# Performance work log

Measured on AMD Instinct MI355X. Metric: run time of the kernel, lower is better.

The kernel has to match this reference:

```python
import jax, jax.numpy as jnp
import numpy as np

B, T, HID, H = 2, 2048, 2048, 8
DK, DV = 256, 512          # head_qk_dim, head_v_dim
CHUNK = 64                 # chunk size used by fused_chunk retention
EPS = 1e-5


def setup_inputs() -> dict:
    key = jax.random.key(0)
    ks = jax.random.split(key, 7)
    s = 0.02  # ~ xavier_uniform with gain 2**-2.5
    return {
        "hidden_states": jax.random.normal(ks[0], (B, T, HID), jnp.float32),
        "Wq": jax.random.normal(ks[1], (HID, H * DK), jnp.float32) * s,
        "Wk": jax.random.normal(ks[2], (HID, H * DK), jnp.float32) * s,
        "Wv": jax.random.normal(ks[3], (HID, H * DV), jnp.float32) * s,
        "Wg": jax.random.normal(ks[4], (HID, H * DV), jnp.float32) * s,
        "Wo": jax.random.normal(ks[5], (H * DV, HID), jnp.float32) * s,
        "g_norm_w": jnp.ones((DV,), jnp.float32),
    }


def _rotary(x):
    # x: [B, T, H, D], non-interleaved rotary over full head dim, base 10000
    d = x.shape[-1]
    inv = 1.0 / (10000.0 ** (jnp.arange(0, d, 2, dtype=jnp.float32) / d))
    fr = jnp.arange(x.shape[1], dtype=jnp.float32)[:, None] * inv  # [T, d/2]
    cos = jnp.cos(fr)[None, :, None, :]
    sin = jnp.sin(fr)[None, :, None, :]
    x1, x2 = jnp.split(x, 2, axis=-1)
    return jnp.concatenate([x1 * cos - x2 * sin, x2 * cos + x1 * sin], axis=-1)


def _retention(q, k, v):
    # q,k: [B,H,T,DK]; v: [B,H,T,DV]; per-head decay gamma_h = 1 - 2^(-5-h)
    gamma = 1.0 - jnp.exp2(-5.0 - jnp.arange(H, dtype=jnp.float32))  # [H]
    q = q * (DK ** -0.5)
    N = T // CHUNK
    qc = q.reshape(B, H, N, CHUNK, DK).transpose(2, 0, 1, 3, 4)  # [N,B,H,C,K]
    kc = k.reshape(B, H, N, CHUNK, DK).transpose(2, 0, 1, 3, 4)
    vc = v.reshape(B, H, N, CHUNK, DV).transpose(2, 0, 1, 3, 4)
    i = jnp.arange(CHUNK, dtype=jnp.float32)
    # intra-chunk causal decay matrix D[h,i,j] = gamma_h^(i-j) for i>=j else 0
    Dm = jnp.where(i[:, None] >= i[None, :],
                   gamma[:, None, None] ** (i[:, None] - i[None, :]), 0.0)  # [H,C,C]
    qd = gamma[:, None] ** (i + 1.0)            # [H,C]: decay applied to q vs carried state
    kd = gamma[:, None] ** (CHUNK - 1.0 - i)    # [H,C]: decay applied to k for state update
    gC = gamma ** CHUNK                          # [H]

    def step(S, qkv):
        qcu, kcu, vcu = qkv  # [B,H,C,K], [B,H,C,K], [B,H,C,V]
        A = jnp.einsum('bhik,bhjk->bhij', qcu, kcu) * Dm[None]
        o_intra = jnp.einsum('bhij,bhjv->bhiv', A, vcu)
        o_inter = jnp.einsum('bhck,bhkv->bhcv', qcu * qd[None, :, :, None], S)
        kv = jnp.einsum('bhck,bhcv->bhkv', kcu * kd[None, :, :, None], vcu)
        S_new = gC[None, :, None, None] * S + kv
        return S_new, o_intra + o_inter

    S0 = jnp.zeros((B, H, DK, DV), jnp.float32)
    _, o = jax.lax.scan(step, S0, (qc, kc, vc))  # o: [N,B,H,C,V]
    return o.transpose(1, 2, 0, 3, 4).reshape(B, H, T, DV)


def reference(hidden_states, Wq, Wk, Wv, Wg, Wo, g_norm_w):
    q = (hidden_states @ Wq).reshape(B, T, H, DK)
    k = (hidden_states @ Wk).reshape(B, T, H, DK)
    v = (hidden_states @ Wv).reshape(B, T, H, DV)
    q = _rotary(q)
    k = _rotary(k)
    o = _retention(q.transpose(0, 2, 1, 3), k.transpose(0, 2, 1, 3),
                   v.transpose(0, 2, 1, 3))          # [B,H,T,DV]
    o = o.transpose(0, 2, 1, 3)                       # [B,T,H,DV]
    g = (hidden_states @ Wg).reshape(B, T, H, DV)
    # fused RMSNorm (per head_v_dim) + swish gate
    o = o * jax.lax.rsqrt(jnp.mean(o * o, axis=-1, keepdims=True) + EPS) * g_norm_w
    o = o * (g * jax.nn.sigmoid(g))
    return o.reshape(B, T, H * DV) @ Wo
```

## Files before the change

kernel.cpp:

```cpp
#include <hip/hip_runtime.h>
#include <cstdint>
#include <cstddef>

typedef __bf16 bf16;
typedef __bf16 bf16x8 __attribute__((ext_vector_type(8)));
typedef float  f32x4  __attribute__((ext_vector_type(4)));

#define MFMA16(a, b, c) __builtin_amdgcn_mfma_f32_16x16x32_bf16((a), (b), (c), 0, 0, 0)

__device__ __forceinline__ void async16(const bf16* g, bf16* l) {
  __builtin_amdgcn_global_load_lds(
      (const __attribute__((address_space(1))) unsigned int*)g,
      (__attribute__((address_space(3))) unsigned int*)l, 16, 0, 0);
}

__global__ __launch_bounds__(256) void k_cast(const float* __restrict__ x, bf16* __restrict__ y) {
  size_t i = ((size_t)blockIdx.x * 256 + threadIdx.x) * 4;
  float4 a = *(const float4*)(x + i);
  union { bf16 h[4]; uint2 u; } pk;
  pk.h[0] = (bf16)a.x; pk.h[1] = (bf16)a.y; pk.h[2] = (bf16)a.z; pk.h[3] = (bf16)a.w;
  *(uint2*)(y + i) = pk.u;
}

__global__ __launch_bounds__(256) void k_wt_all(const float* __restrict__ Wq,
                                                const float* __restrict__ Wk,
                                                const float* __restrict__ Wv,
                                                const float* __restrict__ Wg,
                                                bf16* __restrict__ WT) {
  const int K = 2048;
  __shared__ float tile[32][33];
  int z = blockIdx.z;
  const float* W; bf16* dst; int N;
  if (z == 0)      { W = Wq; dst = WT;                          N = 2048; }
  else if (z == 1) { W = Wk; dst = WT + (size_t)2048 * 2048;    N = 2048; }
  else if (z == 2) { W = Wv; dst = WT + (size_t)4096 * 2048;    N = 4096; }
  else             { W = Wg; dst = WT + (size_t)8192 * 2048;    N = 4096; }
  int n0 = blockIdx.x << 5;
  if (n0 >= N) return;
  int k0 = blockIdx.y << 5;
  int r = threadIdx.x >> 5, c = threadIdx.x & 31;
#pragma unroll
  for (int p = 0; p < 4; p++)
    tile[r + p * 8][c] = W[(size_t)(k0 + r + p * 8) * N + n0 + c];
  __syncthreads();
#pragma unroll
  for (int p = 0; p < 4; p++) {
    int nn = r + p * 8;
    dst[(size_t)(n0 + nn) * K + k0 + c] = (bf16)tile[c][nn];
  }
}

__global__ __launch_bounds__(256) void k_transpose_cast(const float* __restrict__ W,
                                                        bf16* __restrict__ WT, int K, int N) {
  __shared__ float tile[32][33];
  int k0 = blockIdx.y << 5, n0 = blockIdx.x << 5;
  int r = threadIdx.x >> 5, c = threadIdx.x & 31;
#pragma unroll
  for (int p = 0; p < 4; p++)
    tile[r + p * 8][c] = W[(size_t)(k0 + r + p * 8) * N + n0 + c];
  __syncthreads();
#pragma unroll
  for (int p = 0; p < 4; p++) {
    int nn = r + p * 8;
    WT[(size_t)(n0 + nn) * K + k0 + c] = (bf16)tile[c][nn];
  }
}

__global__ __launch_bounds__(256) void k_transpose_bh(const bf16* __restrict__ src,
                                                      bf16* __restrict__ dst, int D) {
  __shared__ bf16 tile[32][33];
  int bh = blockIdx.z;
  int b = bh >> 3, h = bh & 7;
  int d0 = blockIdx.x << 5, t0 = blockIdx.y << 5;
  int r = threadIdx.x >> 5, c = threadIdx.x & 31;
#pragma unroll
  for (int p = 0; p < 4; p++)
    tile[r + p * 8][c] = src[((size_t)((b * 2048 + t0 + r + p * 8) * 8 + h)) * D + d0 + c];
  __syncthreads();
#pragma unroll
  for (int p = 0; p < 4; p++)
    dst[((size_t)(bh * D + d0 + r + p * 8)) * 2048 + t0 + c] = tile[c][r + p * 8];
}

__global__ __launch_bounds__(256) void k_gemm_qkvg(const bf16* __restrict__ A,
                                                   const bf16* __restrict__ Bt,
                                                   bf16* __restrict__ qb, bf16* __restrict__ kb,
                                                   bf16* __restrict__ vbuf, bf16* __restrict__ gb) {
  const int K = 2048;
  __shared__ bf16 a_lds[128 * 64];
  __shared__ bf16 b_lds[128 * 64];
  int tid = threadIdx.x;
  int wave = tid >> 6, lane = tid & 63, quad = lane >> 4, l16 = lane & 15;
  int wr = wave >> 1, wc = wave & 1;
  int m0 = blockIdx.y << 7, n0 = blockIdx.x << 7;
  f32x4 acc[4][4] = {};
  int rl = tid >> 3;
  int sb = (tid & 7) ^ (rl & 7);
  const bf16* ag = A + (size_t)(m0 + rl) * K + sb * 8;
  const bf16* bg = Bt + (size_t)(n0 + rl) * K + sb * 8;
  bf16* al = a_lds + wave * 512;
  bf16* bl = b_lds + wave * 512;
  int sw = (l16 & 7) << 3;
  for (int kt = 0; kt < K; kt += 64) {
#pragma unroll
    for (int i = 0; i < 4; i++) {
      async16(ag + (size_t)i * 32 * K, al + i * 2048);
      async16(bg + (size_t)i * 32 * K, bl + i * 2048);
    }
    ag += 64; bg += 64;
    __syncthreads();
#pragma unroll
    for (int kk = 0; kk < 2; kk++) {
      int bo = ((kk * 4 + quad) << 3) ^ sw;
      bf16x8 af[4], bfv[4];
#pragma unroll
      for (int mt = 0; mt < 4; mt++)
        af[mt] = *(const bf16x8*)&a_lds[(wr * 64 + mt * 16 + l16) * 64 + bo];
#pragma unroll
      for (int nt = 0; nt < 4; nt++)
        bfv[nt] = *(const bf16x8*)&b_lds[(wc * 64 + nt * 16 + l16) * 64 + bo];
#pragma unroll
      for (int mt = 0; mt < 4; mt++)
#pragma unroll
        for (int nt = 0; nt < 4; nt++)
          acc[mt][nt] = MFMA16(af[mt], bfv[nt], acc[mt][nt]);
    }
    __syncthreads();
  }
  bf16* dst; int ldd, c0;
  if (n0 < 2048)       { dst = qb;   ldd = 2048; c0 = n0; }
  else if (n0 < 4096)  { dst = kb;   ldd = 2048; c0 = n0 - 2048; }
  else if (n0 < 8192)  { dst = vbuf; ldd = 4096; c0 = n0 - 4096; }
  else                 { dst = gb;   ldd = 4096; c0 = n0 - 8192; }
#pragma unroll
  for (int mt = 0; mt < 4; mt++)
#pragma unroll
    for (int nt = 0; nt < 4; nt++)
#pragma unroll
      for (int r = 0; r < 4; r++) {
        int row = m0 + wr * 64 + mt * 16 + quad * 4 + r;
        int col = c0 + wc * 64 + nt * 16 + l16;
        dst[(size_t)row * ldd + col] = (bf16)acc[mt][nt][r];
      }
}

__global__ __launch_bounds__(256) void k_gemm_bt(const bf16* __restrict__ A,
                                                 const bf16* __restrict__ Bt,
                                                 float* __restrict__ C, int M, int N, int K) {
  __shared__ bf16 a_lds[128 * 64];
  __shared__ bf16 b_lds[128 * 64];
  int tid = threadIdx.x;
  int wave = tid >> 6, lane = tid & 63, quad = lane >> 4, l16 = lane & 15;
  int wr = wave >> 1, wc = wave & 1;
  int m0 = blockIdx.y << 7, n0 = blockIdx.x << 7;
  f32x4 acc[4][4] = {};
  int rl = tid >> 3;
  int sb = (tid & 7) ^ (rl & 7);
  const bf16* ag = A + (size_t)(m0 + rl) * K + sb * 8;
  const bf16* bg = Bt + (size_t)(n0 + rl) * K + sb * 8;
  bf16* al = a_lds + wave * 512;
  bf16* bl = b_lds + wave * 512;
  int sw = (l16 & 7) << 3;
  for (int kt = 0; kt < K; kt += 64) {
#pragma unroll
    for (int i = 0; i < 4; i++) {
      async16(ag + (size_t)i * 32 * K, al + i * 2048);
      async16(bg + (size_t)i * 32 * K, bl + i * 2048);
    }
    ag += 64; bg += 64;
    __syncthreads();
#pragma unroll
    for (int kk = 0; kk < 2; kk++) {
      int bo = ((kk * 4 + quad) << 3) ^ sw;
      bf16x8 af[4], bfv[4];
#pragma unroll
      for (int mt = 0; mt < 4; mt++)
        af[mt] = *(const bf16x8*)&a_lds[(wr * 64 + mt * 16 + l16) * 64 + bo];
#pragma unroll
      for (int nt = 0; nt < 4; nt++)
        bfv[nt] = *(const bf16x8*)&b_lds[(wc * 64 + nt * 16 + l16) * 64 + bo];
#pragma unroll
      for (int mt = 0; mt < 4; mt++)
#pragma unroll
        for (int nt = 0; nt < 4; nt++)
          acc[mt][nt] = MFMA16(af[mt], bfv[nt], acc[mt][nt]);
    }
    __syncthreads();
  }
#pragma unroll
  for (int mt = 0; mt < 4; mt++)
#pragma unroll
    for (int nt = 0; nt < 4; nt++)
#pragma unroll
      for (int r = 0; r < 4; r++) {
        int row = m0 + wr * 64 + mt * 16 + quad * 4 + r;
        int col = n0 + wc * 64 + nt * 16 + l16;
        C[(size_t)row * N + col] = acc[mt][nt][r];
      }
}

__global__ __launch_bounds__(256) void k_rotary2(bf16* __restrict__ q, bf16* __restrict__ k) {
  int bid = blockIdx.x;
  bf16* x; int kmode;
  if (bid < 16384) { x = q; kmode = 0; }
  else             { x = k; kmode = 1; bid -= 16384; }
  int tid = threadIdx.x;
  int row = bid * 2 + (tid >> 7);
  int j = tid & 127;
  int t = (row >> 3) & 2047;
  int h = row & 7;
  float scale;
  if (kmode) {
    float lg = log2f(1.f - exp2f(-5.f - (float)h));
    scale = exp2f(lg * (float)(63 - (t & 63)));
  } else {
    scale = 0.0625f;
  }
  float inv = exp2f(-0.10381025296522976f * (float)j);
  float ang = (float)t * inv;
  float s, c;
  sincosf(ang, &s, &c);
  size_t base = (size_t)row * 256;
  float x1 = (float)x[base + j], x2 = (float)x[base + j + 128];
  x[base + j]       = (bf16)((x1 * c - x2 * s) * scale);
  x[base + j + 128] = (bf16)((x2 * c + x1 * s) * scale);
}

__global__ __launch_bounds__(256) void k_retention(const bf16* __restrict__ q,
                                                   const bf16* __restrict__ k,
                                                   const bf16* __restrict__ kT,
                                                   const bf16* __restrict__ vT,
                                                   bf16* __restrict__ o0,
                                                   bf16* __restrict__ o1) {
  __shared__ bf16 ktA[2][128 * 64];
  __shared__ bf16 vtA[2][32 * 64];
  __shared__ bf16 StA[32 * 136];

  int gid = blockIdx.x;
  int kh = gid & 1, h = (gid >> 1) & 7, b = (gid >> 4) & 1, vb = gid >> 5;
  int bh = b * 8 + h;
  bf16* oout = kh ? o1 : o0;
  int tid = threadIdx.x, lane = tid & 63, wave = tid >> 6, quad = lane >> 4, l16 = lane & 15;
  float gamma = 1.f - exp2f(-5.f - (float)h);
  float lg = log2f(gamma);
  float gC = exp2f(64.f * lg);
  int iRow = wave * 16 + l16;
  float ei = exp2f(lg * (float)(iRow - 63));
  float qd[4];
#pragma unroll
  for (int r = 0; r < 4; r++) qd[r] = exp2f(lg * (float)(wave * 16 + quad * 4 + r + 1));
  int sw = (l16 & 7) << 3;

  const bf16* qrow = q + ((size_t)(b * 2048) * 8 + h) * 256 + kh * 128;
  const bf16* krow = k + ((size_t)(b * 2048) * 8 + h) * 256 + kh * 128;

  f32x4 S[2][2];
#pragma unroll
  for (int a = 0; a < 2; a++)
#pragma unroll
    for (int bb = 0; bb < 2; bb++) S[a][bb] = (f32x4){0.f, 0.f, 0.f, 0.f};

  auto stage = [&](int t0, int p) {
#pragma unroll 1
    for (int s = wave; s < 20; s += 4) {
      if (s < 16) {
        int kd = s * 8 + (lane >> 3);
        int blk = (lane & 7) ^ (kd & 7);
        async16(kT + ((size_t)(bh * 256 + kh * 128 + kd)) * 2048 + t0 + blk * 8,
                &ktA[p][s * 512]);
      } else {
        int i = s - 16, vd = i * 8 + (lane >> 3);
        int blk = (lane & 7) ^ (vd & 7);
        async16(vT + ((size_t)(bh * 512 + vb * 32 + vd)) * 2048 + t0 + blk * 8,
                &vtA[p][i * 512]);
      }
    }
  };

  stage(0, 0);

  for (int n = 0; n < 32; n++) {
    int p = n & 1, t0 = n * 64;
#pragma unroll
    for (int a = 0; a < 2; a++)
#pragma unroll
      for (int bb = 0; bb < 2; bb++) {
        int k0 = wave * 32 + a * 16 + quad * 4;
        int vc = bb * 16 + l16;
        f32x4 s = S[a][bb];
        union { bf16 hh[4]; unsigned long long u; } pkk;
        pkk.hh[0] = (bf16)s[0]; pkk.hh[1] = (bf16)s[1];
        pkk.hh[2] = (bf16)s[2]; pkk.hh[3] = (bf16)s[3];
        *(unsigned long long*)&StA[vc * 136 + k0] = pkk.u;
      }
    __syncthreads();
    if (n < 31) stage(t0 + 64, 1 - p);

    bf16x8 qf[4];
#pragma unroll
    for (int kk = 0; kk < 4; kk++)
      qf[kk] = *(const bf16x8*)(qrow + (size_t)(t0 + iRow) * 2048 + kk * 32 + quad * 8);

    f32x4 Dt[4];
#pragma unroll
    for (int jt = 0; jt < 4; jt++) {
      Dt[jt] = (f32x4){0.f, 0.f, 0.f, 0.f};
#pragma unroll
      for (int kk = 0; kk < 4; kk++) {
        bf16x8 kf = *(const bf16x8*)(krow + (size_t)(t0 + jt * 16 + l16) * 2048 + kk * 32 + quad * 8);
        Dt[jt] = MFMA16(kf, qf[kk], Dt[jt]);
      }
    }
    unsigned pkA[4][2];
#pragma unroll
    for (int jt = 0; jt < 4; jt++) {
      int j0 = jt * 16 + quad * 4;
      union { bf16 hh[2]; unsigned u; } p0, p1;
      p0.hh[0] = (bf16)((iRow >= j0 + 0) ? Dt[jt][0] * ei : 0.f);
      p0.hh[1] = (bf16)((iRow >= j0 + 1) ? Dt[jt][1] * ei : 0.f);
      p1.hh[0] = (bf16)((iRow >= j0 + 2) ? Dt[jt][2] * ei : 0.f);
      p1.hh[1] = (bf16)((iRow >= j0 + 3) ? Dt[jt][3] * ei : 0.f);
      pkA[jt][0] = p0.u; pkA[jt][1] = p1.u;
    }
    int s0b = ((((quad & 1) << 5) + l16) << 2);
    int s1b = s0b + 64;
    bool hi = (quad >> 1) != 0;
    bf16x8 afA[2];
#pragma unroll
    for (int kk = 0; kk < 2; kk++) {
      unsigned x00 = __builtin_amdgcn_ds_bpermute(s0b, (int)pkA[2 * kk][0]);
      unsigned x01 = __builtin_amdgcn_ds_bpermute(s0b, (int)pkA[2 * kk][1]);
      unsigned x10 = __builtin_amdgcn_ds_bpermute(s0b, (int)pkA[2 * kk + 1][0]);
      unsigned x11 = __builtin_amdgcn_ds_bpermute(s0b, (int)pkA[2 * kk + 1][1]);
      unsigned y00 = __builtin_amdgcn_ds_bpermute(s1b, (int)pkA[2 * kk][0]);
      unsigned y01 = __builtin_amdgcn_ds_bpermute(s1b, (int)pkA[2 * kk][1]);
      unsigned y10 = __builtin_amdgcn_ds_bpermute(s1b, (int)pkA[2 * kk + 1][0]);
      unsigned y11 = __builtin_amdgcn_ds_bpermute(s1b, (int)pkA[2 * kk + 1][1]);
      union { unsigned u[4]; bf16x8 v; } rr;
      rr.u[0] = hi ? x10 : x00;
      rr.u[1] = hi ? x11 : x01;
      rr.u[2] = hi ? y10 : y00;
      rr.u[3] = hi ? y11 : y01;
      afA[kk] = rr.v;
    }

    f32x4 oacc[2];
#pragma unroll
    for (int nt = 0; nt < 2; nt++) {
      oacc[nt] = (f32x4){0.f, 0.f, 0.f, 0.f};
#pragma unroll
      for (int kk = 0; kk < 4; kk++) {
        bf16x8 stf = *(const bf16x8*)&StA[(nt * 16 + l16) * 136 + kk * 32 + quad * 8];
        oacc[nt] = MFMA16(qf[kk], stf, oacc[nt]);
      }
    }
#pragma unroll
    for (int nt = 0; nt < 2; nt++)
#pragma unroll
      for (int r = 0; r < 4; r++) oacc[nt][r] *= qd[r];

    bf16x8 vtf[2][2];
#pragma unroll
    for (int nt = 0; nt < 2; nt++)
#pragma unroll
      for (int kk = 0; kk < 2; kk++)
        vtf[nt][kk] = *(const bf16x8*)&vtA[p][(nt * 16 + l16) * 64 + ((((kk * 4 + quad) << 3)) ^ sw)];
#pragma unroll
    for (int nt = 0; nt < 2; nt++)
#pragma unroll
      for (int kk = 0; kk < 2; kk++)
        oacc[nt] = MFMA16(afA[kk], vtf[nt][kk], oacc[nt]);

#pragma unroll
    for (int nt = 0; nt < 2; nt++)
#pragma unroll
      for (int r = 0; r < 4; r++) {
        int row = t0 + wave * 16 + quad * 4 + r;
        int col = vb * 32 + nt * 16 + l16;
        oout[((size_t)((b * 2048 + row) * 8 + h)) * 512 + col] = (bf16)oacc[nt][r];
      }

#pragma unroll
    for (int a = 0; a < 2; a++) {
      bf16x8 ktf[2];
#pragma unroll
      for (int kk = 0; kk < 2; kk++)
        ktf[kk] = *(const bf16x8*)&ktA[p][(wave * 32 + a * 16 + l16) * 64 + ((((kk * 4 + quad) << 3)) ^ sw)];
#pragma unroll
      for (int bb = 0; bb < 2; bb++) {
        f32x4 cc = S[a][bb] * gC;
#pragma unroll
        for (int kk = 0; kk < 2; kk++) cc = MFMA16(ktf[kk], vtf[bb][kk], cc);
        S[a][bb] = cc;
      }
    }
    __syncthreads();
  }
}

__global__ __launch_bounds__(256) void k_normgate(const bf16* __restrict__ o0,
                                                  const bf16* __restrict__ o1,
                                                  const bf16* __restrict__ g,
                                                  const float* __restrict__ gw,
                                                  bf16* __restrict__ og) {
  int tid = threadIdx.x, lane = tid & 63;
  size_t row = (size_t)blockIdx.x * 4 + (tid >> 6);
  size_t base = row * 512;
  float vv[8];
  float ss = 0.f;
#pragma unroll
  for (int hh = 0; hh < 2; hh++) {
    int col = hh * 256 + lane * 4;
    union { bf16 h[4]; uint2 u; } a, b2;
    a.u = *(const uint2*)(o0 + base + col);
    b2.u = *(const uint2*)(o1 + base + col);
#pragma unroll
    for (int jj = 0; jj < 4; jj++) {
      float v = (float)a.h[jj] + (float)b2.h[jj];
      vv[hh * 4 + jj] = v;
      ss += v * v;
    }
  }
#pragma unroll
  for (int off = 1; off < 64; off <<= 1) ss += __shfl_xor(ss, off, 64);
  float rinv = rsqrtf(ss * (1.0f / 512.0f) + 1e-5f);
#pragma unroll
  for (int hh = 0; hh < 2; hh++) {
    int col = hh * 256 + lane * 4;
    union { bf16 h[4]; uint2 u; } gp;
    gp.u = *(const uint2*)(g + base + col);
    union { bf16 h[4]; uint2 u; } op;
#pragma unroll
    for (int jj = 0; jj < 4; jj++) {
      float gg = (float)gp.h[jj];
      float y = vv[hh * 4 + jj] * rinv * gw[col + jj] * (gg / (1.f + expf(-gg)));
      op.h[jj] = (bf16)y;
    }
    *(uint2*)(og + base + col) = op.u;
  }
}

extern "C" void kernel_launch(void* const* d_in, const int* in_sizes, int n_in,
                              void* d_out, int out_size, void* d_ws, size_t ws_size,
                              hipStream_t stream) {
  (void)in_sizes; (void)n_in; (void)out_size; (void)ws_size;
  const float* hs = (const float*)d_in[0];
  const float* Wq = (const float*)d_in[1];
  const float* Wk = (const float*)d_in[2];
  const float* Wv = (const float*)d_in[3];
  const float* Wg = (const float*)d_in[4];
  const float* Wo = (const float*)d_in[5];
  const float* gw = (const float*)d_in[6];
  float* out = (float*)d_out;

  char* ws = (char*)d_ws;
  const size_t MB = 1024 * 1024;
  bf16* hid = (bf16*)(ws + 0);
  bf16* WT  = (bf16*)(ws + 16 * MB);
  bf16* qb  = (bf16*)(ws + 64 * MB);
  bf16* kb  = (bf16*)(ws + 80 * MB);
  bf16* vbuf= (bf16*)(ws + 96 * MB);
  bf16* gb  = (bf16*)(ws + 128 * MB);
  bf16* kT  = (bf16*)(ws + 160 * MB);
  bf16* vT  = (bf16*)(ws + 176 * MB);
  bf16* o0  = (bf16*)(ws + 0);
  bf16* o1  = (bf16*)(ws + 32 * MB);
  bf16* og  = (bf16*)(ws + 160 * MB);
  bf16* WoT = (bf16*)(ws + 192 * MB);

  k_cast<<<8192, 256, 0, stream>>>(hs, hid);
  k_wt_all<<<dim3(128, 64, 4), 256, 0, stream>>>(Wq, Wk, Wv, Wg, WT);

  k_gemm_qkvg<<<dim3(96, 32), 256, 0, stream>>>(hid, WT, qb, kb, vbuf, gb);

  k_rotary2<<<32768, 256, 0, stream>>>(qb, kb);

  k_transpose_bh<<<dim3(8, 64, 16), 256, 0, stream>>>(kb, kT, 256);
  k_transpose_bh<<<dim3(16, 64, 16), 256, 0, stream>>>(vbuf, vT, 512);

  k_retention<<<512, 256, 0, stream>>>(qb, kb, kT, vT, o0, o1);

  k_transpose_cast<<<dim3(64, 128), 256, 0, stream>>>(Wo, WoT, 4096, 2048);
  k_normgate<<<8192, 256, 0, stream>>>(o0, o1, gb, gw, og);
  k_gemm_bt<<<dim3(16, 32), 256, 0, stream>>>(og, WoT, out, 4096, 2048, 4096);
}
```

Before: 717.3 us.

## Stage q and k chunks in LDS and drop double buffering in retention

The retention kernel now loads the q and k chunk tiles into swizzled shared memory with async global-to-LDS copies, instead of having each wave read q/k fragments straight from global memory. The k and v transposed buffers become single-buffered, and the prefetch of the next chunk moves to after the trailing barrier. The intent is to replace scattered global fragment loads with coalesced async copies, and to make room in LDS for the extra tiles. The cost is that the next chunk's load no longer overlaps the current chunk's compute, so load latency is exposed on every iteration.

New measurement: 662.8 us. 1.08x faster.

```diff
diff --git a/kernel.cpp b/kernel.cpp
--- a/kernel.cpp
+++ b/kernel.cpp
@@ -232,8 +232,10 @@
                                                    const bf16* __restrict__ vT,
                                                    bf16* __restrict__ o0,
                                                    bf16* __restrict__ o1) {
-  __shared__ bf16 ktA[2][128 * 64];
-  __shared__ bf16 vtA[2][32 * 64];
+  __shared__ bf16 qA[64 * 128];
+  __shared__ bf16 kA[64 * 128];
+  __shared__ bf16 ktA[128 * 64];
+  __shared__ bf16 vtA[32 * 64];
   __shared__ bf16 StA[32 * 136];
 
   int gid = blockIdx.x;
@@ -251,36 +253,43 @@
   for (int r = 0; r < 4; r++) qd[r] = exp2f(lg * (float)(wave * 16 + quad * 4 + r + 1));
   int sw = (l16 & 7) << 3;
 
-  const bf16* qrow = q + ((size_t)(b * 2048) * 8 + h) * 256 + kh * 128;
-  const bf16* krow = k + ((size_t)(b * 2048) * 8 + h) * 256 + kh * 128;
-
   f32x4 S[2][2];
 #pragma unroll
   for (int a = 0; a < 2; a++)
 #pragma unroll
     for (int bb = 0; bb < 2; bb++) S[a][bb] = (f32x4){0.f, 0.f, 0.f, 0.f};
 
-  auto stage = [&](int t0, int p) {
+  auto stage = [&](int t0) {
 #pragma unroll 1
-    for (int s = wave; s < 20; s += 4) {
+    for (int s = wave; s < 52; s += 4) {
       if (s < 16) {
-        int kd = s * 8 + (lane >> 3);
+        int c = s * 4 + (lane >> 4);
+        int blk = (lane & 15) ^ (c & 7);
+        async16(q + (((size_t)((b * 2048 + t0 + c) * 8 + h)) << 8) + kh * 128 + blk * 8,
+                &qA[s * 512]);
+      } else if (s < 32) {
+        int i = s - 16, c = i * 4 + (lane >> 4);
+        int blk = (lane & 15) ^ (c & 7);
+        async16(k + (((size_t)((b * 2048 + t0 + c) * 8 + h)) << 8) + kh * 128 + blk * 8,
+                &kA[i * 512]);
+      } else if (s < 48) {
+        int i = s - 32, kd = i * 8 + (lane >> 3);
         int blk = (lane & 7) ^ (kd & 7);
         async16(kT + ((size_t)(bh * 256 + kh * 128 + kd)) * 2048 + t0 + blk * 8,
-                &ktA[p][s * 512]);
+                &ktA[i * 512]);
       } else {
-        int i = s - 16, vd = i * 8 + (lane >> 3);
+        int i = s - 48, vd = i * 8 + (lane >> 3);
         int blk = (lane & 7) ^ (vd & 7);
         async16(vT + ((size_t)(bh * 512 + vb * 32 + vd)) * 2048 + t0 + blk * 8,
-                &vtA[p][i * 512]);
+                &vtA[i * 512]);
       }
     }
   };
 
-  stage(0, 0);
+  stage(0);
 
   for (int n = 0; n < 32; n++) {
-    int p = n & 1, t0 = n * 64;
+    int t0 = n * 64;
 #pragma unroll
     for (int a = 0; a < 2; a++)
 #pragma unroll
@@ -294,12 +303,11 @@
         *(unsigned long long*)&StA[vc * 136 + k0] = pkk.u;
       }
     __syncthreads();
-    if (n < 31) stage(t0 + 64, 1 - p);
 
     bf16x8 qf[4];
 #pragma unroll
     for (int kk = 0; kk < 4; kk++)
-      qf[kk] = *(const bf16x8*)(qrow + (size_t)(t0 + iRow) * 2048 + kk * 32 + quad * 8);
+      qf[kk] = *(const bf16x8*)&qA[iRow * 128 + ((((kk * 4 + quad) << 3)) ^ sw)];
 
     f32x4 Dt[4];
 #pragma unroll
@@ -307,7 +315,7 @@
       Dt[jt] = (f32x4){0.f, 0.f, 0.f, 0.f};
 #pragma unroll
       for (int kk = 0; kk < 4; kk++) {
-        bf16x8 kf = *(const bf16x8*)(krow + (size_t)(t0 + jt * 16 + l16) * 2048 + kk * 32 + quad * 8);
+        bf16x8 kf = *(const bf16x8*)&kA[(jt * 16 + l16) * 128 + ((((kk * 4 + quad) << 3)) ^ sw)];
         Dt[jt] = MFMA16(kf, qf[kk], Dt[jt]);
       }
     }
@@ -364,7 +372,7 @@
     for (int nt = 0; nt < 2; nt++)
 #pragma unroll
       for (int kk = 0; kk < 2; kk++)
-        vtf[nt][kk] = *(const bf16x8*)&vtA[p][(nt * 16 + l16) * 64 + ((((kk * 4 + quad) << 3)) ^ sw)];
+        vtf[nt][kk] = *(const bf16x8*)&vtA[(nt * 16 + l16) * 64 + ((((kk * 4 + quad) << 3)) ^ sw)];
 #pragma unroll
     for (int nt = 0; nt < 2; nt++)
 #pragma unroll
@@ -385,7 +393,7 @@
       bf16x8 ktf[2];
 #pragma unroll
       for (int kk = 0; kk < 2; kk++)
-        ktf[kk] = *(const bf16x8*)&ktA[p][(wave * 32 + a * 16 + l16) * 64 + ((((kk * 4 + quad) << 3)) ^ sw)];
+        ktf[kk] = *(const bf16x8*)&ktA[(wave * 32 + a * 16 + l16) * 64 + ((((kk * 4 + quad) << 3)) ^ sw)];
 #pragma unroll
       for (int bb = 0; bb < 2; bb++) {
         f32x4 cc = S[a][bb] * gC;
@@ -395,6 +403,7 @@
       }
     }
     __syncthreads();
+    if (n < 31) stage(t0 + 64);
   }
 }
 
```
